# Performance work log

Hardware: AMD Instinct MI355X
Metric: run time of the kernel (lower is better)

The kernel has to match this reference:

```python
import jax, jax.numpy as jnp
import numpy as np

RC = 6.0
N_BASIS = 32
WIDTH = 0.25
N_CONV = 3
MU = jnp.linspace(0.5, 6.0, N_BASIS)  # Gaussian RBF centers ('distances')


def ssp(x):
    # shifted softplus activation (SchNet-style)
    return jax.nn.softplus(x) - jnp.log(2.0)


def setup_inputs() -> dict:
    key = jax.random.key(0)
    ks = jax.random.split(key, 20)
    B, N, F, K = 16, 128, 128, 32
    S = 16  # n_species
    coords = jax.random.normal(ks[0], (B, N, 3), dtype=jnp.float32) * 4.0
    species = jax.random.randint(ks[1], (B, N), 0, S)
    g = lambda k, shape, fan: jax.random.normal(k, shape, dtype=jnp.float32) / np.sqrt(fan)
    return {
        "coords": coords,
        "species": species,
        "emb_table": g(ks[2], (S, F), 1.0),
        # convolve_net: K -> F -> F
        "Wc1": g(ks[3], (K, F), K), "bc1": jnp.zeros((F,)),
        "Wc2": g(ks[4], (F, F), F), "bc2": jnp.zeros((F,)),
        # update_net: F -> F -> F
        "Wu1": g(ks[5], (F, F), F), "bu1": jnp.zeros((F,)),
        "Wu2": g(ks[6], (F, F), F), "bu2": jnp.zeros((F,)),
        # pool_net: F -> 64 -> 8 (isotropic coefficients)
        "Wp1": g(ks[7], (F, 64), F), "bp1": jnp.zeros((64,)),
        "Wp2": g(ks[8], (64, 8), 64), "bp2": jnp.zeros((8,)),
        # edge_net: 2F -> F -> 16 (anisotropic coefficients); split as Wi/Wj
        "Wei": g(ks[9], (F, F), 2 * F), "Wej": g(ks[10], (F, F), 2 * F),
        "be1": jnp.zeros((F,)),
        "We2": g(ks[11], (F, 16), F), "be2": jnp.zeros((16,)),
    }


def reference(coords, species, emb_table,
              Wc1, bc1, Wc2, bc2,
              Wu1, bu1, Wu2, bu2,
              Wp1, bp1, Wp2, bp2,
              Wei, Wej, be1, We2, be2):
    B, N, _ = coords.shape
    # --- MolecularEmbedding ---
    h = emb_table[species]                                   # [B,N,F]
    # --- pairwise geometry (shared across conv iterations; coords fixed) ---
    diff = coords[:, :, None, :] - coords[:, None, :, :]      # [B,N,N,3]
    d2 = jnp.sum(diff * diff, axis=-1)                        # [B,N,N]
    d = jnp.sqrt(jnp.where(d2 > 0, d2, 1.0))                  # safe sqrt (diag masked out)
    eye = jnp.eye(N, dtype=bool)
    mask = ((d < RC) & ~eye).astype(h.dtype)[..., None]       # [B,N,N,1]
    rbf = jnp.exp(-((d[..., None] - MU) ** 2) / (2.0 * WIDTH ** 2))  # [B,N,N,K]
    # convolve_net: RBF -> continuous filter weights [B,N,N,F]
    Wf = (ssp(rbf @ Wc1 + bc1) @ Wc2 + bc2) * mask
    # --- n_convolutions x MessagePassing ---
    for _ in range(N_CONV):
        m = jnp.einsum('bijf,bjf->bif', Wf, h)                # gather-weight-scatter
        h = h + (ssp(m @ Wu1 + bu1) @ Wu2 + bu2)              # update_net (residual)
    # --- NodePool -> c_iso [B,N,8] ---
    c_iso = ssp(h @ Wp1 + bp1) @ Wp2 + bp2
    # --- EdgePool -> c_aniso [B,N,N,16], summed over neighbor axis ---
    pre_i = h @ Wei                                           # [B,N,F]
    pre_j = h @ Wej                                           # [B,N,F]
    hid = ssp(pre_i[:, :, None, :] + pre_j[:, None, :, :] + be1)  # [B,N,N,F]
    c_aniso = (hid @ We2 + be2) * mask                        # [B,N,N,16]
    return c_iso, c_aniso.sum(2)
```

## Files before the change

kernel.cpp:

```cpp
#include <hip/hip_runtime.h>


#define LN2F 0.69314718055994531f

__device__ __forceinline__ float sspf(float x) {
  float e = __expf(-fabsf(x));
  return fmaxf(x, 0.0f) + __logf(1.0f + e) - LN2F;
}
__device__ __forceinline__ unsigned int f2bf(float x) {
  unsigned int u = __float_as_uint(x);
  return (u + 0x7fffu + ((u >> 16) & 1u)) >> 16;
}
__device__ __forceinline__ float bflo(unsigned int u) { return __uint_as_float(u << 16); }
__device__ __forceinline__ float bfhi(unsigned int u) { return __uint_as_float(u & 0xffff0000u); }

__global__ __launch_bounds__(256) void prep_kernel(
    const float* __restrict__ coords,
    const float* __restrict__ Wc1, const float* __restrict__ bc1,
    const float* __restrict__ Wc2, const float* __restrict__ bc2,
    unsigned int* __restrict__ tb16,
    unsigned int* __restrict__ ent, int* __restrict__ cnt) {
  int t = threadIdx.x;
  if (blockIdx.x < 1024) {
    __shared__ int wc[4];
    int node = blockIdx.x * 2 + (t >> 7);
    int j = t & 127;
    int b = node >> 7, i = node & 127;
    const float* cb = coords + (b << 7) * 3;
    float dx = cb[i*3+0] - cb[j*3+0];
    float dy = cb[i*3+1] - cb[j*3+1];
    float dz = cb[i*3+2] - cb[j*3+2];
    float d  = sqrtf(dx*dx + dy*dy + dz*dz);
    bool valid = (d < 6.0f) && (j != i);
    int k = 4096;
    if (valid) { k = (int)(d * (4096.0f/6.0f)); if (k > 4095) k = 4095; }
    unsigned long long bal = __ballot(valid);
    int lane = t & 63, w = t >> 6;
    if (lane == 0) wc[w] = (int)__popcll(bal);
    __syncthreads();
    int ii = t >> 7;
    int nn = wc[2*ii] + wc[2*ii+1];
    int base = ((w & 1) ? wc[w-1] : 0) + (int)__popcll(bal & ((1ull << lane) - 1ull));
    if (valid) ent[node*128 + base] = (unsigned int)(j | (k << 7));
    int nnp = (nn + 15) & ~15;
    if (nnp > 128) nnp = 128;
    if (j >= nn && j < nnp) ent[node*128 + j] = (4096u << 7);
    if (j == 0) cnt[node] = nn | (nnp << 16);
  } else {
    __shared__ float rbf[8][32];
    __shared__ float hid[8][128];
    int tb = (int)blockIdx.x - 1024;
    int t0 = tb * 8;
    { int tt = t >> 5, kk = t & 31;
      float d = (float)(t0 + tt) * (6.0f/4096.0f) + 0.5f * (6.0f/4096.0f);
      float mu = 0.5f + (float)kk * (5.5f/31.0f);
      float z = d - mu;
      rbf[tt][kk] = __expf(-8.0f * z * z); }
    __syncthreads();
    int f = t & 127, sub = t >> 7;
    float s0 = bc1[f], s1 = s0, s2 = s0, s3 = s0;
    int r0 = sub * 4;
    for (int kk = 0; kk < 32; kk++) {
      float wv = Wc1[kk*128 + f];
      s0 += rbf[r0+0][kk]*wv; s1 += rbf[r0+1][kk]*wv;
      s2 += rbf[r0+2][kk]*wv; s3 += rbf[r0+3][kk]*wv;
    }
    hid[r0+0][f] = sspf(s0); hid[r0+1][f] = sspf(s1);
    hid[r0+2][f] = sspf(s2); hid[r0+3][f] = sspf(s3);
    __syncthreads();
    float o0 = bc2[f], o1 = o0, o2 = o0, o3 = o0;
    for (int g = 0; g < 128; g++) {
      float wv = Wc2[g*128 + f];
      o0 += hid[r0+0][g]*wv; o1 += hid[r0+1][g]*wv;
      o2 += hid[r0+2][g]*wv; o3 += hid[r0+3][g]*wv;
    }
    unsigned int l0 = f2bf(o0), l1 = f2bf(o1), l2 = f2bf(o2), l3 = f2bf(o3);
    unsigned int p0 = (unsigned int)__shfl_xor((int)l0, 1);
    unsigned int p1 = (unsigned int)__shfl_xor((int)l1, 1);
    unsigned int p2 = (unsigned int)__shfl_xor((int)l2, 1);
    unsigned int p3 = (unsigned int)__shfl_xor((int)l3, 1);
    if ((f & 1) == 0) {
      int fw = f >> 1;
      tb16[(t0+r0+0)*64 + fw] = l0 | (p0 << 16);
      tb16[(t0+r0+1)*64 + fw] = l1 | (p1 << 16);
      tb16[(t0+r0+2)*64 + fw] = l2 | (p2 << 16);
      tb16[(t0+r0+3)*64 + fw] = l3 | (p3 << 16);
    }
    if (tb == 0 && t < 64) tb16[4096*64 + t] = 0u;
  }
}

template<bool SRC_EMB, bool LAST>
__global__ __launch_bounds__(512) void conv_t(
    const float* __restrict__ h_in, const unsigned int* __restrict__ hbf_in,
    float* __restrict__ h_out, unsigned int* __restrict__ hbf_out,
    const int* __restrict__ species, const float* __restrict__ emb,
    const unsigned int* __restrict__ tb16, const unsigned int* __restrict__ ent,
    const int* __restrict__ cnt,
    const float* __restrict__ Wu1, const float* __restrict__ bu1,
    const float* __restrict__ Wu2, const float* __restrict__ bu2,
    const float* __restrict__ Wp1, const float* __restrict__ bp1,
    const float* __restrict__ Wp2, const float* __restrict__ bp2,
    const float* __restrict__ Wei, const float* __restrict__ Wej,
    float* __restrict__ pre_i, unsigned int* __restrict__ prejbf,
    float* __restrict__ out) {
  __shared__ unsigned int hsh[8192];
  __shared__ unsigned int ent_s[4][128];
  __shared__ float mred[8][128];
  __shared__ float m_s[4][128];
  __shared__ float red[4][4][128];
  __shared__ float u1_s[4][128];
  __shared__ int nn_s[4];
  int t = threadIdx.x;
  int node0 = blockIdx.x * 4;
  int b = blockIdx.x >> 5;

  if constexpr (SRC_EMB) {
    const int* spb = species + (b << 7);
    for (int c = 0; c < 16; c++) {
      int idx = c*512 + t;
      int j = idx >> 6, f2 = idx & 63;
      float2 v = *(const float2*)(emb + spb[j]*128 + 2*f2);
      hsh[idx] = (f2bf(v.y) << 16) | f2bf(v.x);
    }
  } else {
    const unsigned int* hb = hbf_in + b * 8192;
    for (int c = 0; c < 16; c++) hsh[c*512 + t] = hb[c*512 + t];
  }
  { int ii = t >> 7, f = t & 127;
    ent_s[ii][f] = ent[(node0 + ii)*128 + f]; }
  if (t < 4) nn_s[t] = cnt[node0 + t];
  __syncthreads();

  int w = t >> 6, lane = t & 63;
  int ii = w >> 1, par = w & 1;
  int nnp = nn_s[ii] >> 16;
  float a0 = 0.f, a1 = 0.f, b0 = 0.f, b1 = 0.f;
  float c0 = 0.f, c1 = 0.f, d0 = 0.f, d1 = 0.f;
  for (int e = par; e < nnp; e += 16) {
    unsigned int u0 = ent_s[ii][e],      u1 = ent_s[ii][e + 2];
    unsigned int u2 = ent_s[ii][e + 4],  u3 = ent_s[ii][e + 6];
    unsigned int u4 = ent_s[ii][e + 8],  u5 = ent_s[ii][e + 10];
    unsigned int u6 = ent_s[ii][e + 12], u7 = ent_s[ii][e + 14];
    unsigned int t0 = tb16[(u0 >> 7)*64 + lane];
    unsigned int t1 = tb16[(u1 >> 7)*64 + lane];
    unsigned int t2 = tb16[(u2 >> 7)*64 + lane];
    unsigned int t3 = tb16[(u3 >> 7)*64 + lane];
    unsigned int t4 = tb16[(u4 >> 7)*64 + lane];
    unsigned int t5 = tb16[(u5 >> 7)*64 + lane];
    unsigned int t6 = tb16[(u6 >> 7)*64 + lane];
    unsigned int t7 = tb16[(u7 >> 7)*64 + lane];
    unsigned int h0 = hsh[(u0 & 127)*64 + lane];
    unsigned int h1 = hsh[(u1 & 127)*64 + lane];
    unsigned int h2 = hsh[(u2 & 127)*64 + lane];
    unsigned int h3 = hsh[(u3 & 127)*64 + lane];
    unsigned int h4 = hsh[(u4 & 127)*64 + lane];
    unsigned int h5 = hsh[(u5 & 127)*64 + lane];
    unsigned int h6 = hsh[(u6 & 127)*64 + lane];
    unsigned int h7 = hsh[(u7 & 127)*64 + lane];
    a0 += bflo(t0) * bflo(h0); a1 += bfhi(t0) * bfhi(h0);
    b0 += bflo(t1) * bflo(h1); b1 += bfhi(t1) * bfhi(h1);
    c0 += bflo(t2) * bflo(h2); c1 += bfhi(t2) * bfhi(h2);
    d0 += bflo(t3) * bflo(h3); d1 += bfhi(t3) * bfhi(h3);
    a0 += bflo(t4) * bflo(h4); a1 += bfhi(t4) * bfhi(h4);
    b0 += bflo(t5) * bflo(h5); b1 += bfhi(t5) * bfhi(h5);
    c0 += bflo(t6) * bflo(h6); c1 += bfhi(t6) * bfhi(h6);
    d0 += bflo(t7) * bflo(h7); d1 += bfhi(t7) * bfhi(h7);
  }
  a0 += b0 + c0 + d0; a1 += b1 + c1 + d1;
  *(float2*)&mred[w][2*lane] = make_float2(a0, a1);
  __syncthreads();
  { int i2 = t >> 7, f = t & 127;
    m_s[i2][f] = mred[2*i2][f] + mred[2*i2+1][f]; }
  __syncthreads();

  int g = t & 127, q = t >> 7;
  {
    float p0=0,p1=0,p2=0,p3=0;
    for (int f = q*32; f < q*32 + 32; f++) {
      float wv = Wu1[f*128 + g];
      p0 += m_s[0][f]*wv; p1 += m_s[1][f]*wv; p2 += m_s[2][f]*wv; p3 += m_s[3][f]*wv;
    }
    red[q][0][g]=p0; red[q][1][g]=p1; red[q][2][g]=p2; red[q][3][g]=p3;
  }
  __syncthreads();
  { int i2 = t >> 7, gg = t & 127;
    u1_s[i2][gg] = sspf(red[0][i2][gg]+red[1][i2][gg]+red[2][i2][gg]+red[3][i2][gg] + bu1[gg]); }
  __syncthreads();
  {
    float p0=0,p1=0,p2=0,p3=0;
    for (int f = q*32; f < q*32 + 32; f++) {
      float wv = Wu2[f*128 + g];
      p0 += u1_s[0][f]*wv; p1 += u1_s[1][f]*wv; p2 += u1_s[2][f]*wv; p3 += u1_s[3][f]*wv;
    }
    red[q][0][g]=p0; red[q][1][g]=p1; red[q][2][g]=p2; red[q][3][g]=p3;
  }
  __syncthreads();
  { int i2 = t >> 7, o = t & 127;
    int node = node0 + i2;
    float delta = red[0][i2][o]+red[1][i2][o]+red[2][i2][o]+red[3][i2][o] + bu2[o];
    float base;
    if constexpr (SRC_EMB) base = emb[species[node]*128 + o];
    else                   base = h_in[node*128 + o];
    float hf = base + delta;
    if constexpr (!LAST) {
      h_out[node*128 + o] = hf;
      unsigned int lo = f2bf(hf);
      unsigned int hi = (unsigned int)__shfl_xor((int)lo, 1);
      if ((o & 1) == 0) hbf_out[node*64 + (o >> 1)] = lo | (hi << 16);
    } else {
      u1_s[i2][o] = hf;
    }
  }
  if constexpr (LAST) {
    __syncthreads();
    float (*hs)[128]     = u1_s;
    float (*redp)[4][64] = reinterpret_cast<float (*)[4][64]>(red);
    float (*us)[64]      = reinterpret_cast<float (*)[64]>(m_s);
    int gp = t & 63, qp = t >> 6;
    float p0=0,p1=0,p2=0,p3=0;
    for (int f = qp*16; f < qp*16 + 16; f++) {
      float wv = Wp1[f*64 + gp];
      p0 += hs[0][f]*wv; p1 += hs[1][f]*wv; p2 += hs[2][f]*wv; p3 += hs[3][f]*wv;
    }
    redp[qp][0][gp]=p0; redp[qp][1][gp]=p1; redp[qp][2][gp]=p2; redp[qp][3][gp]=p3;
    __syncthreads();
    if (t < 256) {
      int i4 = t >> 6, gg = t & 63;
      float s = bp1[gg];
      for (int q2 = 0; q2 < 8; q2++) s += redp[q2][i4][gg];
      us[i4][gg] = sspf(s);
    }
    __syncthreads();
    if (t < 32) {
      int i4 = t >> 3, o = t & 7;
      float v = bp2[o];
      for (int gg = 0; gg < 64; gg++) v += us[i4][gg] * Wp2[gg*8 + o];
      out[(node0 + i4)*8 + o] = v;
    }
    int o = t & 127, sel = (t >> 7) & 1, duo = t >> 8;
    const float* W = sel ? Wej : Wei;
    float q0 = 0.f, q1 = 0.f;
    for (int f = 0; f < 128; f++) {
      float wv = W[f*128 + o];
      q0 += hs[2*duo][f]*wv; q1 += hs[2*duo+1][f]*wv;
    }
    if (sel == 0) {
      pre_i[(node0 + 2*duo)*128 + o]     = q0;
      pre_i[(node0 + 2*duo + 1)*128 + o] = q1;
    } else {
      unsigned int l0 = f2bf(q0), l1 = f2bf(q1);
      unsigned int h0 = (unsigned int)__shfl_xor((int)l0, 1);
      unsigned int h1 = (unsigned int)__shfl_xor((int)l1, 1);
      if ((o & 1) == 0) {
        prejbf[(node0 + 2*duo)*64 + (o >> 1)]     = l0 | (h0 << 16);
        prejbf[(node0 + 2*duo + 1)*64 + (o >> 1)] = l1 | (h1 << 16);
      }
    }
  }
}

__global__ __launch_bounds__(512) void edgepool_kernel(
    const float* __restrict__ pre_i, const unsigned int* __restrict__ prejbf,
    const unsigned int* __restrict__ ent, const int* __restrict__ cnt,
    const float* __restrict__ be1, const float* __restrict__ We2,
    const float* __restrict__ be2, float* __restrict__ out) {
  __shared__ unsigned int pjs[8192];
  __shared__ unsigned int ent_s[4][128];
  __shared__ float pis[4][128];
  __shared__ float sred[8][128];
  __shared__ float s_s[4][128];
  __shared__ float r2[4][8][16];
  __shared__ int nn_s[4];
  int t = threadIdx.x;
  int node0 = blockIdx.x * 4;
  int b = blockIdx.x >> 5;
  const unsigned int* pjb = prejbf + b * 8192;
  for (int c = 0; c < 16; c++) pjs[c*512 + t] = pjb[c*512 + t];
  { int ii = t >> 7, f = t & 127;
    pis[ii][f] = pre_i[(node0 + ii)*128 + f] + be1[f];
    ent_s[ii][f] = ent[(node0 + ii)*128 + f]; }
  if (t < 4) nn_s[t] = cnt[node0 + t] & 0xffff;
  __syncthreads();
  int w = t >> 6, lane = t & 63;
  int ii = w >> 1, par = w & 1;
  float pia = pis[ii][2*lane];
  float pib = pis[ii][2*lane + 1];
  int nn = nn_s[ii];
  float a0 = 0.f, a1 = 0.f;
  for (int e = par; e < nn; e += 2) {
    unsigned int u = ent_s[ii][e];
    int j = u & 127;
    unsigned int hv = pjs[j*64 + lane];
    a0 += sspf(pia + bflo(hv));
    a1 += sspf(pib + bfhi(hv));
  }
  *(float2*)&sred[w][2*lane] = make_float2(a0, a1);
  __syncthreads();
  { int i2 = t >> 7, f = t & 127;
    s_s[i2][f] = sred[2*i2][f] + sred[2*i2+1][f]; }
  __syncthreads();
  { int i2 = t >> 7, o = t & 15, seg = (t >> 4) & 7;
    float p = 0.f;
    for (int f = seg*16; f < seg*16 + 16; f++) p += s_s[i2][f] * We2[f*16 + o];
    r2[i2][seg][o] = p; }
  __syncthreads();
  if (t < 64) {
    int i2 = t >> 4, o = t & 15;
    float v = be2[o] * (float)nn_s[i2];
    for (int seg = 0; seg < 8; seg++) v += r2[i2][seg][o];
    out[(node0 + i2)*16 + o] = v;
  }
}

extern "C" void kernel_launch(void* const* d_in, const int* in_sizes, int n_in,
                              void* d_out, int out_size, void* d_ws, size_t ws_size,
                              hipStream_t stream) {
  const float* coords = (const float*)d_in[0];
  const int*   species= (const int*)  d_in[1];
  const float* emb    = (const float*)d_in[2];
  const float* Wc1    = (const float*)d_in[3];
  const float* bc1    = (const float*)d_in[4];
  const float* Wc2    = (const float*)d_in[5];
  const float* bc2    = (const float*)d_in[6];
  const float* Wu1    = (const float*)d_in[7];
  const float* bu1    = (const float*)d_in[8];
  const float* Wu2    = (const float*)d_in[9];
  const float* bu2    = (const float*)d_in[10];
  const float* Wp1    = (const float*)d_in[11];
  const float* bp1    = (const float*)d_in[12];
  const float* Wp2    = (const float*)d_in[13];
  const float* bp2    = (const float*)d_in[14];
  const float* Wei    = (const float*)d_in[15];
  const float* Wej    = (const float*)d_in[16];
  const float* be1    = (const float*)d_in[17];
  const float* We2    = (const float*)d_in[18];
  const float* be2    = (const float*)d_in[19];
  float* out = (float*)d_out;

  float* wsf = (float*)d_ws;
  unsigned int* tb16   = (unsigned int*)wsf;
  float*        h_a    = wsf + 524416;
  float*        h_b    = wsf + 786560;
  float*        pre_i  = wsf + 1048704;
  unsigned int* hbf_a  = (unsigned int*)(wsf + 1310848);
  unsigned int* hbf_b  = (unsigned int*)(wsf + 1441920);
  unsigned int* prejbf = (unsigned int*)(wsf + 1572992);
  unsigned int* ent    = (unsigned int*)(wsf + 1704064);
  int*          cnt    = (int*)(wsf + 1966208);
  (void)in_sizes; (void)n_in; (void)out_size; (void)ws_size;

  prep_kernel<<<1536, 256, 0, stream>>>(coords, Wc1, bc1, Wc2, bc2, tb16, ent, cnt);
  conv_t<true, false><<<512, 512, 0, stream>>>(
      nullptr, nullptr, h_b, hbf_b, species, emb, tb16, ent, cnt,
      Wu1, bu1, Wu2, bu2,
      nullptr, nullptr, nullptr, nullptr, nullptr, nullptr, nullptr, nullptr, nullptr);
  conv_t<false, false><<<512, 512, 0, stream>>>(
      h_b, hbf_b, h_a, hbf_a, species, emb, tb16, ent, cnt,
      Wu1, bu1, Wu2, bu2,
      nullptr, nullptr, nullptr, nullptr, nullptr, nullptr, nullptr, nullptr, nullptr);
  conv_t<false, true><<<512, 512, 0, stream>>>(
      h_a, hbf_a, nullptr, nullptr, species, emb, tb16, ent, cnt,
      Wu1, bu1, Wu2, bu2,
      Wp1, bp1, Wp2, bp2, Wei, Wej, pre_i, prejbf, out);
  edgepool_kernel<<<512, 512, 0, stream>>>(pre_i, prejbf, ent, cnt, be1, We2, be2,
                                           out + 16384);
}
```

Baseline: 56.57 us.

## Drop LDS staging of neighbor features, swizzle blocks for L2 locality, unroll edgepool

The conv and edgepool kernels no longer copy a whole molecule's 32KB of bf16 features into shared memory. They gather neighbor rows straight from global memory, and block indices are remapped so consecutive blocks land on different XCDs while blocks of the same molecule share an L2. The embedding lookup moves into prep_kernel, which writes the initial h and bf16 h, so all conv launches use one template path. Edgepool is unrolled by four over padded edge lists and subtracts the padding contributions analytically. This removes the per-block LDS fill cost and raises occupancy, at the risk of higher global/L2 latency on the gathers.

```diff
diff --git a/kernel.cpp b/kernel.cpp
--- a/kernel.cpp
+++ b/kernel.cpp
@@ -15,15 +15,19 @@
 __device__ __forceinline__ float bfhi(unsigned int u) { return __uint_as_float(u & 0xffff0000u); }
 
 __global__ __launch_bounds__(256) void prep_kernel(
-    const float* __restrict__ coords,
+    const float* __restrict__ coords, const int* __restrict__ species,
+    const float* __restrict__ emb,
     const float* __restrict__ Wc1, const float* __restrict__ bc1,
     const float* __restrict__ Wc2, const float* __restrict__ bc2,
-    unsigned int* __restrict__ tb16,
+    unsigned int* __restrict__ tb16, float* __restrict__ h_a,
+    unsigned int* __restrict__ hbf_a,
     unsigned int* __restrict__ ent, int* __restrict__ cnt) {
   int t = threadIdx.x;
   if (blockIdx.x < 1024) {
     __shared__ int wc[4];
-    int node = blockIdx.x * 2 + (t >> 7);
+    int blk = (int)blockIdx.x;
+    int Lb = ((blk & 7) << 7) | (blk >> 3);
+    int node = Lb * 2 + (t >> 7);
     int j = t & 127;
     int b = node >> 7, i = node & 127;
     const float* cb = coords + (b << 7) * 3;
@@ -46,6 +50,11 @@
     if (nnp > 128) nnp = 128;
     if (j >= nn && j < nnp) ent[node*128 + j] = (4096u << 7);
     if (j == 0) cnt[node] = nn | (nnp << 16);
+    float hv = emb[species[node]*128 + j];
+    h_a[node*128 + j] = hv;
+    unsigned int lo = f2bf(hv);
+    unsigned int hi = (unsigned int)__shfl_xor((int)lo, 1);
+    if ((j & 1) == 0) hbf_a[node*64 + (j >> 1)] = lo | (hi << 16);
   } else {
     __shared__ float rbf[8][32];
     __shared__ float hid[8][128];
@@ -90,11 +99,10 @@
   }
 }
 
-template<bool SRC_EMB, bool LAST>
+template<bool LAST>
 __global__ __launch_bounds__(512) void conv_t(
     const float* __restrict__ h_in, const unsigned int* __restrict__ hbf_in,
     float* __restrict__ h_out, unsigned int* __restrict__ hbf_out,
-    const int* __restrict__ species, const float* __restrict__ emb,
     const unsigned int* __restrict__ tb16, const unsigned int* __restrict__ ent,
     const int* __restrict__ cnt,
     const float* __restrict__ Wu1, const float* __restrict__ bu1,
@@ -104,7 +112,6 @@
     const float* __restrict__ Wei, const float* __restrict__ Wej,
     float* __restrict__ pre_i, unsigned int* __restrict__ prejbf,
     float* __restrict__ out) {
-  __shared__ unsigned int hsh[8192];
   __shared__ unsigned int ent_s[4][128];
   __shared__ float mred[8][128];
   __shared__ float m_s[4][128];
@@ -112,21 +119,12 @@
   __shared__ float u1_s[4][128];
   __shared__ int nn_s[4];
   int t = threadIdx.x;
-  int node0 = blockIdx.x * 4;
-  int b = blockIdx.x >> 5;
-
-  if constexpr (SRC_EMB) {
-    const int* spb = species + (b << 7);
-    for (int c = 0; c < 16; c++) {
-      int idx = c*512 + t;
-      int j = idx >> 6, f2 = idx & 63;
-      float2 v = *(const float2*)(emb + spb[j]*128 + 2*f2);
-      hsh[idx] = (f2bf(v.y) << 16) | f2bf(v.x);
-    }
-  } else {
-    const unsigned int* hb = hbf_in + b * 8192;
-    for (int c = 0; c < 16; c++) hsh[c*512 + t] = hb[c*512 + t];
-  }
+  int blk = (int)blockIdx.x;
+  int Lb = ((blk & 7) << 6) | (blk >> 3);
+  int node0 = Lb * 4;
+  int b = Lb >> 5;
+  const unsigned int* hb = hbf_in + (b << 13);
+
   { int ii = t >> 7, f = t & 127;
     ent_s[ii][f] = ent[(node0 + ii)*128 + f]; }
   if (t < 4) nn_s[t] = cnt[node0 + t];
@@ -150,14 +148,14 @@
     unsigned int t5 = tb16[(u5 >> 7)*64 + lane];
     unsigned int t6 = tb16[(u6 >> 7)*64 + lane];
     unsigned int t7 = tb16[(u7 >> 7)*64 + lane];
-    unsigned int h0 = hsh[(u0 & 127)*64 + lane];
-    unsigned int h1 = hsh[(u1 & 127)*64 + lane];
-    unsigned int h2 = hsh[(u2 & 127)*64 + lane];
-    unsigned int h3 = hsh[(u3 & 127)*64 + lane];
-    unsigned int h4 = hsh[(u4 & 127)*64 + lane];
-    unsigned int h5 = hsh[(u5 & 127)*64 + lane];
-    unsigned int h6 = hsh[(u6 & 127)*64 + lane];
-    unsigned int h7 = hsh[(u7 & 127)*64 + lane];
+    unsigned int h0 = hb[(u0 & 127)*64 + lane];
+    unsigned int h1 = hb[(u1 & 127)*64 + lane];
+    unsigned int h2 = hb[(u2 & 127)*64 + lane];
+    unsigned int h3 = hb[(u3 & 127)*64 + lane];
+    unsigned int h4 = hb[(u4 & 127)*64 + lane];
+    unsigned int h5 = hb[(u5 & 127)*64 + lane];
+    unsigned int h6 = hb[(u6 & 127)*64 + lane];
+    unsigned int h7 = hb[(u7 & 127)*64 + lane];
     a0 += bflo(t0) * bflo(h0); a1 += bfhi(t0) * bfhi(h0);
     b0 += bflo(t1) * bflo(h1); b1 += bfhi(t1) * bfhi(h1);
     c0 += bflo(t2) * bflo(h2); c1 += bfhi(t2) * bfhi(h2);
@@ -199,10 +197,7 @@
   { int i2 = t >> 7, o = t & 127;
     int node = node0 + i2;
     float delta = red[0][i2][o]+red[1][i2][o]+red[2][i2][o]+red[3][i2][o] + bu2[o];
-    float base;
-    if constexpr (SRC_EMB) base = emb[species[node]*128 + o];
-    else                   base = h_in[node*128 + o];
-    float hf = base + delta;
+    float hf = h_in[node*128 + o] + delta;
     if constexpr (!LAST) {
       h_out[node*128 + o] = hf;
       unsigned int lo = f2bf(hf);
@@ -265,7 +260,6 @@
     const unsigned int* __restrict__ ent, const int* __restrict__ cnt,
     const float* __restrict__ be1, const float* __restrict__ We2,
     const float* __restrict__ be2, float* __restrict__ out) {
-  __shared__ unsigned int pjs[8192];
   __shared__ unsigned int ent_s[4][128];
   __shared__ float pis[4][128];
   __shared__ float sred[8][128];
@@ -273,27 +267,41 @@
   __shared__ float r2[4][8][16];
   __shared__ int nn_s[4];
   int t = threadIdx.x;
-  int node0 = blockIdx.x * 4;
-  int b = blockIdx.x >> 5;
-  const unsigned int* pjb = prejbf + b * 8192;
-  for (int c = 0; c < 16; c++) pjs[c*512 + t] = pjb[c*512 + t];
+  int blk = (int)blockIdx.x;
+  int Lb = ((blk & 7) << 6) | (blk >> 3);
+  int node0 = Lb * 4;
+  int b = Lb >> 5;
+  const unsigned int* pjb = prejbf + (b << 13);
   { int ii = t >> 7, f = t & 127;
     pis[ii][f] = pre_i[(node0 + ii)*128 + f] + be1[f];
     ent_s[ii][f] = ent[(node0 + ii)*128 + f]; }
-  if (t < 4) nn_s[t] = cnt[node0 + t] & 0xffff;
+  if (t < 4) nn_s[t] = cnt[node0 + t];
   __syncthreads();
   int w = t >> 6, lane = t & 63;
   int ii = w >> 1, par = w & 1;
   float pia = pis[ii][2*lane];
   float pib = pis[ii][2*lane + 1];
-  int nn = nn_s[ii];
+  int cw = nn_s[ii];
+  int nn = cw & 0xffff, nnp = cw >> 16;
   float a0 = 0.f, a1 = 0.f;
-  for (int e = par; e < nn; e += 2) {
-    unsigned int u = ent_s[ii][e];
-    int j = u & 127;
-    unsigned int hv = pjs[j*64 + lane];
-    a0 += sspf(pia + bflo(hv));
-    a1 += sspf(pib + bfhi(hv));
+  for (int e = par; e < nnp; e += 8) {
+    unsigned int u0 = ent_s[ii][e],     u1 = ent_s[ii][e + 2];
+    unsigned int u2 = ent_s[ii][e + 4], u3 = ent_s[ii][e + 6];
+    unsigned int v0 = pjb[(u0 & 127)*64 + lane];
+    unsigned int v1 = pjb[(u1 & 127)*64 + lane];
+    unsigned int v2 = pjb[(u2 & 127)*64 + lane];
+    unsigned int v3 = pjb[(u3 & 127)*64 + lane];
+    a0 += sspf(pia + bflo(v0)) + sspf(pia + bflo(v1))
+        + sspf(pia + bflo(v2)) + sspf(pia + bflo(v3));
+    a1 += sspf(pib + bfhi(v0)) + sspf(pib + bfhi(v1))
+        + sspf(pib + bfhi(v2)) + sspf(pib + bfhi(v3));
+  }
+  int npad = nnp - nn;
+  int cp = (npad >> 1) + (((npad & 1) != 0 && (nn & 1) == par) ? 1 : 0);
+  if (cp > 0) {
+    unsigned int v0 = pjb[lane];
+    a0 -= (float)cp * sspf(pia + bflo(v0));
+    a1 -= (float)cp * sspf(pib + bfhi(v0));
   }
   *(float2*)&sred[w][2*lane] = make_float2(a0, a1);
   __syncthreads();
@@ -307,7 +315,7 @@
   __syncthreads();
   if (t < 64) {
     int i2 = t >> 4, o = t & 15;
-    float v = be2[o] * (float)nn_s[i2];
+    float v = be2[o] * (float)(nn_s[i2] & 0xffff);
     for (int seg = 0; seg < 8; seg++) v += r2[i2][seg][o];
     out[(node0 + i2)*16 + o] = v;
   }
@@ -350,17 +358,18 @@
   int*          cnt    = (int*)(wsf + 1966208);
   (void)in_sizes; (void)n_in; (void)out_size; (void)ws_size;
 
-  prep_kernel<<<1536, 256, 0, stream>>>(coords, Wc1, bc1, Wc2, bc2, tb16, ent, cnt);
-  conv_t<true, false><<<512, 512, 0, stream>>>(
-      nullptr, nullptr, h_b, hbf_b, species, emb, tb16, ent, cnt,
+  prep_kernel<<<1536, 256, 0, stream>>>(coords, species, emb, Wc1, bc1, Wc2, bc2,
+                                        tb16, h_a, hbf_a, ent, cnt);
+  conv_t<false><<<512, 512, 0, stream>>>(
+      h_a, hbf_a, h_b, hbf_b, tb16, ent, cnt,
       Wu1, bu1, Wu2, bu2,
       nullptr, nullptr, nullptr, nullptr, nullptr, nullptr, nullptr, nullptr, nullptr);
-  conv_t<false, false><<<512, 512, 0, stream>>>(
-      h_b, hbf_b, h_a, hbf_a, species, emb, tb16, ent, cnt,
+  conv_t<false><<<512, 512, 0, stream>>>(
+      h_b, hbf_b, h_a, hbf_a, tb16, ent, cnt,
       Wu1, bu1, Wu2, bu2,
       nullptr, nullptr, nullptr, nullptr, nullptr, nullptr, nullptr, nullptr, nullptr);
-  conv_t<false, true><<<512, 512, 0, stream>>>(
-      h_a, hbf_a, nullptr, nullptr, species, emb, tb16, ent, cnt,
+  conv_t<true><<<512, 512, 0, stream>>>(
+      h_a, hbf_a, nullptr, nullptr, tb16, ent, cnt,
       Wu1, bu1, Wu2, bu2,
       Wp1, bp1, Wp2, bp2, Wei, Wej, pre_i, prejbf, out);
   edgepool_kernel<<<512, 512, 0, stream>>>(pre_i, prejbf, ent, cnt, be1, We2, be2,
```

New measurement: 53.21 us (median of 3 runs). -6.0%, faster.
